# Performance work log

Measured on AMD Instinct MI355X. Metric: run time of the kernel, lower is better.

Reference implementation:

```python
import jax, jax.numpy as jnp
import numpy as np

K, T, RHO, V, TH, EH, S, B = 50, 50, 300, 20000, 800, 200, 10, 256
DELTA = 0.005
LOG_DELTA = float(np.log(DELTA))
EPS = 1e-6


def setup_inputs() -> dict:
    key = jax.random.key(0)
    ks = jax.random.split(key, 32)
    f32 = jnp.float32
    rn = lambda i, shp, s=0.02: jax.random.normal(ks[i], shp, f32) * s
    inp = {
        "unique_tokens": jax.random.randint(ks[0], (100,), 0, V),
        "bows": jax.random.uniform(ks[1], (B, V), f32),
        "normalized_bows": jax.random.uniform(ks[2], (B, V), f32),
        "times": jax.random.randint(ks[3], (B,), 0, T),
        "sources": jax.random.randint(ks[4], (B,), 0, S),
        "rnn_inp": jax.random.normal(ks[5], (S, T, V), f32),
        "num_docs": 100000,
        # learned parameters
        "mu_q_alpha": rn(6, (K, T, RHO), 1.0),
        "logsigma_q_alpha": rn(7, (K, T, RHO), 0.1),
        "rho_W": rn(8, (V, RHO)),                 # Linear(rho_size -> vocab, no bias)
        "W1": rn(9, (TH, V + K)), "b1": jnp.zeros((TH,), f32),
        "W2": rn(10, (TH, TH)), "b2": jnp.zeros((TH,), f32),
        "mu_th_W": rn(11, (K, TH)), "mu_th_b": jnp.zeros((K,), f32),
        "ls_th_W": rn(12, (K, TH)), "ls_th_b": jnp.zeros((K,), f32),
        "eta_map_W": rn(13, (EH, V)), "eta_map_b": jnp.zeros((EH,), f32),
        "lstm_Wih": rn(14, (4 * EH, EH)), "lstm_Whh": rn(15, (4 * EH, EH)),
        "lstm_bih": jnp.zeros((4 * EH,), f32), "lstm_bhh": jnp.zeros((4 * EH,), f32),
        "mu_eta_W": rn(16, (K, EH + K)), "mu_eta_b": jnp.zeros((K,), f32),
        "ls_eta_W": rn(17, (K, EH + K)), "ls_eta_b": jnp.zeros((K,), f32),
        "cls_W": rn(18, (S, K)), "cls_b": jnp.zeros((S,), f32),
    }
    return inp


def _lstm(x_seq, Wih, Whh, bih, bhh):
    # x_seq: [T, S, EH]; torch gate order i,f,g,o
    def step(carry, x):
        h, c = carry
        z = x @ Wih.T + bih + h @ Whh.T + bhh
        i, f, g, o = jnp.split(z, 4, axis=-1)
        c = jax.nn.sigmoid(f) * c + jax.nn.sigmoid(i) * jnp.tanh(g)
        h = jax.nn.sigmoid(o) * jnp.tanh(c)
        return (h, c), h
    h0 = jnp.zeros((x_seq.shape[1], Whh.shape[1]), x_seq.dtype)
    _, out = jax.lax.scan(step, (h0, h0), x_seq)
    return out  # [T, S, EH]


def reference(unique_tokens, bows, normalized_bows, times, sources, rnn_inp, num_docs,
              mu_q_alpha, logsigma_q_alpha, rho_W, W1, b1, W2, b2,
              mu_th_W, mu_th_b, ls_th_W, ls_th_b, eta_map_W, eta_map_b,
              lstm_Wih, lstm_Whh, lstm_bih, lstm_bhh,
              mu_eta_W, mu_eta_b, ls_eta_W, ls_eta_b, cls_W, cls_b):
    # eval-mode semantics: reparameterize returns mu, dropout off
    bsz = bows.shape[0]
    coeff = num_docs / bsz

    # ---- alpha: eval-mode alphas_t == mu_q_alpha[:, t, :]; KL vectorized ----
    mu_a, ls_a = mu_q_alpha, logsigma_q_alpha  # [K, T, RHO]
    kl_a0 = 0.5 * jnp.sum((jnp.exp(ls_a[:, 0]) + mu_a[:, 0] ** 2) / (1.0 + EPS) - 1.0 - ls_a[:, 0])
    diff = mu_a[:, 1:] - mu_a[:, :-1]
    kl_at = 0.5 * jnp.sum((jnp.exp(ls_a[:, 1:]) + diff ** 2) / (DELTA + EPS) - 1.0 + LOG_DELTA - ls_a[:, 1:])
    kl_alpha = kl_a0 + kl_at
    alphas = jnp.transpose(mu_a, (1, 0, 2))  # [T, K, RHO]

    # ---- eta: LSTM over time (vmapped over sources as batch), then recurrence ----
    mapped = jnp.einsum('stv,hv->sth', rnn_inp, eta_map_W) + eta_map_b  # [S, T, EH]
    lstm_out = _lstm(jnp.transpose(mapped, (1, 0, 2)), lstm_Wih, lstm_Whh, lstm_bih, lstm_bhh)  # [T, S, EH]

    inp0 = jnp.concatenate([lstm_out[0], jnp.zeros((S, K), lstm_out.dtype)], axis=-1)
    mu0 = inp0 @ mu_eta_W.T + mu_eta_b
    ls0 = inp0 @ ls_eta_W.T + ls_eta_b  # no clipping at t=0 in original
    kl0 = 0.5 * jnp.sum((jnp.exp(ls0) + mu0 ** 2) / (1.0 + EPS) - 1.0 - ls0)

    def eta_step(carry, out_t):
        eta_prev, kl = carry
        inp_t = jnp.concatenate([out_t, eta_prev], axis=-1)
        mu_t = inp_t @ mu_eta_W.T + mu_eta_b
        ls_t = jnp.clip(inp_t @ ls_eta_W.T + ls_eta_b, -10.0, 10.0)
        kl_t = 0.5 * jnp.sum((jnp.exp(ls_t) + (mu_t - eta_prev) ** 2) / (DELTA + EPS) - 1.0 + LOG_DELTA - ls_t)
        return (mu_t, kl + kl_t), mu_t
    (_, kl_rest), etas_rest = jax.lax.scan(eta_step, (mu0, jnp.float32(0.0)), lstm_out[1:])
    etas = jnp.transpose(jnp.concatenate([mu0[None], etas_rest], axis=0), (1, 0, 2))  # [S, T, K]
    kl_eta = kl0 + kl_rest

    # ---- theta ----
    eta_std = etas[sources, times]  # [B, K]
    h = jax.nn.relu(jnp.concatenate([normalized_bows, eta_std], axis=1) @ W1.T + b1)
    h = jax.nn.relu(h @ W2.T + b2)
    mu_t = h @ mu_th_W.T + mu_th_b
    ls_t = jnp.clip(h @ ls_th_W.T + ls_th_b, -10.0, 10.0)
    theta = jax.nn.softmax(mu_t, axis=-1)
    kl_theta = (0.5 * jnp.sum((jnp.exp(ls_t) + (mu_t - eta_std) ** 2) / (1.0 + EPS) - 1.0 - ls_t)) * coeff

    # ---- beta and NLL ----
    logit = jnp.einsum('tkr,vr->tkv', alphas, rho_W)
    beta = jax.nn.softmax(logit, axis=-1)        # [T, K, V]
    beta_d = beta[times]                         # [B, K, V]
    loglik = jnp.log(jnp.einsum('bk,bkv->bv', theta, beta_d))
    nll = -jnp.sum(loglik * bows) * coeff

    # ---- source prediction loss (sum-reduced cross entropy) ----
    logits = theta @ cls_W.T + cls_b
    logp = jax.nn.log_softmax(logits, axis=-1)
    pred_loss = -jnp.sum(jnp.take_along_axis(logp, sources[:, None], axis=1)) * coeff

    nelbo = nll + kl_alpha + kl_eta + kl_theta + pred_loss
    return (nelbo, nll, kl_alpha, kl_eta, kl_theta, pred_loss)
```

## Files before the change

kernel.cpp:

```cpp
#include <hip/hip_runtime.h>

typedef unsigned int u32;
typedef unsigned short ushort_t;

#define NTOP 50
#define NT_T 50
#define NRHO 300
#define NVOC 20000
#define NTH 800
#define NEH 200
#define NSRC 10
#define NBAT 256

#define OFF_SCAL     0
#define OFF_MAPPED   16
#define OFF_HPRE     100016
#define OFF_H2       304816
#define OFF_Z        509616
#define OFF_DOCCNT   512120
#define OFF_DOCLIST  512176
#define MEMSET_BYTES ((size_t)524976 * 4)
#define OFF_XW       524976
#define OFF_BIAS2    924976
#define OFF_ETAS     925776
#define OFF_WCOEF    950776
#define OFF_W1E      963576
#define OFF_WHH_H    1003576
#define OFF_ETAWH    1083576
#define OFF_H1B      1096376
#define OFF_MAPB     1198776
#define OFF_WIHB     1256120
#define OFF_W2B      1356472
#define OFF_ALPHAB   1714872
#define OFF_RHOB     2124472
#define OFF_NBB      5339832
#define OFF_W1B      7899832
#define OFF_RNNB     16859832
#define OFF_EMWB     21979832
#define OFF_LOGITH   7899832

typedef _Float16 h2v __attribute__((ext_vector_type(2)));
typedef __bf16 bf16x8 __attribute__((ext_vector_type(8)));
typedef float f32x4 __attribute__((ext_vector_type(4)));

#define REP25(M) M(0) M(1) M(2) M(3) M(4) M(5) M(6) M(7) M(8) M(9) M(10) M(11) M(12) \
                 M(13) M(14) M(15) M(16) M(17) M(18) M(19) M(20) M(21) M(22) M(23) M(24)
#define REP7(M) M(0) M(1) M(2) M(3) M(4) M(5) M(6)

__device__ inline float dot2u(u32 a, u32 b, float c){
  h2v ha = __builtin_bit_cast(h2v, a), hb = __builtin_bit_cast(h2v, b);
#if __has_builtin(__builtin_amdgcn_fdot2)
  return __builtin_amdgcn_fdot2(ha, hb, c, false);
#else
  return c + (float)ha.x*(float)hb.x + (float)ha.y*(float)hb.y;
#endif
}

__device__ inline u32 packh2(float lo, float hi){
  h2v h; h.x = (_Float16)lo; h.y = (_Float16)hi;
  return __builtin_bit_cast(u32, h);
}

__device__ inline ushort_t f2bf(float f){
  u32 u = __builtin_bit_cast(u32, f);
  u = (u + 0x7FFFu + ((u >> 16) & 1u)) >> 16;
  return (ushort_t)u;
}

__device__ inline float fast_sig(float x){ return 1.f/(1.f + __expf(-x)); }
__device__ inline float fast_tanh(float x){ float e = __expf(2.f*x); return 1.f - 2.f/(e + 1.f); }

__device__ __forceinline__ void gl2lds16(const void* g, void* l){
  __builtin_amdgcn_global_load_lds((__attribute__((address_space(1))) void*)g,
                                   (__attribute__((address_space(3))) void*)l,
                                   16, 0, 0);
}

__device__ inline void blockReduceAdd(float v, float* red, float* target){
  int tid = threadIdx.x;
  red[tid] = v; __syncthreads();
  for (int o = blockDim.x >> 1; o > 0; o >>= 1){
    if (tid < o) red[tid] += red[tid + o];
    __syncthreads();
  }
  if (tid == 0) atomicAdd(target, red[0]);
}

template<int LDSRC, int MREAL, int KUSED, int KP16>
__device__ inline void conv_row16(const float* __restrict__ src, ushort_t* __restrict__ dst, int i)
{
  int row = i / KP16, cc = i - row*KP16;
  int c = cc*16;
  ushort_t* d = dst + ((size_t)row*KP16 + cc)*16;
  float v[16];
  const float* sr = src + (size_t)row*LDSRC + c;
  if (row < MREAL && c + 16 <= KUSED){
    #pragma unroll
    for (int j = 0; j < 16; j++) v[j] = sr[j];
  } else {
    #pragma unroll
    for (int j = 0; j < 16; j++){
      float x = 0.f;
      if (row < MREAL && c + j < KUSED) x = sr[j];
      v[j] = x;
    }
  }
  ushort_t o[16];
  #pragma unroll
  for (int j = 0; j < 16; j++) o[j] = f2bf(v[j]);
  *(uint4*)d = *(uint4*)o;
  *(uint4*)(d + 8) = *(uint4*)(o + 8);
}

#define P0 64
#define P1 128
#define P2 288
#define P3 416
#define P4 864
#define P5 1120
#define P6 1248
#define P7 1256
#define P8 1272
#define P9 1528
__global__ __launch_bounds__(256) void k_mega(
    const float* __restrict__ whh,
    const float* __restrict__ muEW, const float* __restrict__ lsEW,
    const float* __restrict__ bih, const float* __restrict__ bhh,
    const float* __restrict__ wih, const float* __restrict__ emapB,
    const float* __restrict__ W1, const int* __restrict__ times,
    const float* __restrict__ muq, const float* __restrict__ lsq,
    const float* __restrict__ rho, const float* __restrict__ nb,
    const float* __restrict__ rnn, const float* __restrict__ emapW,
    const float* __restrict__ W2f, float* __restrict__ W)
{
  int b = blockIdx.x, tid = threadIdx.x;
  __shared__ float red[256];
  if (b < P0){
    u32* whhH = (u32*)(W + OFF_WHH_H);
    u32* etaWH = (u32*)(W + OFF_ETAWH);
    for (int idx = b*256 + tid; idx < 133856; idx += P0*256){
      if (idx < 80000){
        int j = idx/100; int i = idx - j*100;
        whhH[idx] = packh2(whh[j*200 + 2*i], whh[j*200 + 2*i + 1]);
      } else if (idx < 92800){
        int d = idx - 80000; int q = d >> 7; int i = d & 127;
        u32 v = 0u;
        if (i < 125){
          const float* src = (q < 50) ? (muEW + q*250) : (lsEW + (q-50)*250);
          v = packh2(src[2*i], src[2*i+1]);
        }
        etaWH[d] = v;
      } else if (idx < 93600){
        int j = idx - 92800;
        float acc = bih[j] + bhh[j];
        const float* wr = wih + (size_t)j*200;
        #pragma unroll 4
        for (int k = 0; k < 200; k++) acc += emapB[k]*wr[k];
        W[OFF_BIAS2 + j] = acc;
      } else if (idx < 133600){
        int d = idx - 93600; int j = d/50; int k = d - j*50;
        W[OFF_W1E + d] = W1[(size_t)j*20050 + 20000 + k];
      } else {
        int bb = idx - 133600; int t = times[bb];
        int* docCnt = (int*)(W + OFF_DOCCNT);
        int* docList = (int*)(W + OFF_DOCLIST);
        int pos = atomicAdd(&docCnt[t], 1);
        docList[t*256 + pos] = bb;
      }
    }
  } else if (b < P1){
    ushort_t* dst = (ushort_t*)(W + OFF_ALPHAB);
    for (int idx = (b-P0)*256 + tid; idx < 102400; idx += (P1-P0)*256){
      int row = idx / 40, c = (idx - row*40) << 3;
      ushort_t out[8];
      const float* src = nullptr;
      if (row < 2500){ int t = row/50, k = row - t*50; src = muq + (size_t)k*15000 + t*300; }
      #pragma unroll
      for (int j = 0; j < 8; j++){
        int r = c + j;
        float v = (src && r < 300) ? src[r] : 0.f;
        out[j] = f2bf(v);
      }
      *(uint4*)(dst + (size_t)row*320 + c) = *(uint4*)out;
    }
  } else if (b < P2){
    ushort_t* dst = (ushort_t*)(W + OFF_RHOB);
    #pragma unroll 2
    for (int i = (b-P1)*256 + tid; i < 20096*20; i += (P2-P1)*256)
      conv_row16<300, 20000, 300, 20>(rho, dst, i);
  } else if (b < P3){
    ushort_t* dst = (ushort_t*)(W + OFF_NBB);
    #pragma unroll 2
    for (int i = (b-P2)*256 + tid; i < 256*1250; i += (P3-P2)*256)
      conv_row16<20000, 256, 20000, 1250>(nb, dst, i);
  } else if (b < P4){
    ushort_t* dst = (ushort_t*)(W + OFF_W1B);
    #pragma unroll 2
    for (int i = (b-P3)*256 + tid; i < 896*1250; i += (P4-P3)*256)
      conv_row16<20050, 800, 20000, 1250>(W1, dst, i);
  } else if (b < P5){
    ushort_t* dst = (ushort_t*)(W + OFF_RNNB);
    #pragma unroll 2
    for (int i = (b-P4)*256 + tid; i < 512*1250; i += (P5-P4)*256)
      conv_row16<20000, 500, 20000, 1250>(rnn, dst, i);
  } else if (b < P6){
    ushort_t* dst = (ushort_t*)(W + OFF_EMWB);
    #pragma unroll 2
    for (int i = (b-P5)*256 + tid; i < 256*1250; i += (P6-P5)*256)
      conv_row16<20000, 200, 20000, 1250>(emapW, dst, i);
  } else if (b < P7){
    ushort_t* dst = (ushort_t*)(W + OFF_WIHB);
    #pragma unroll 2
    for (int i = (b-P6)*256 + tid; i < 896*14; i += (P7-P6)*256)
      conv_row16<200, 800, 200, 14>(wih, dst, i);
  } else if (b < P8){
    ushort_t* dst = (ushort_t*)(W + OFF_W2B);
    #pragma unroll 2
    for (int i = (b-P7)*256 + tid; i < 896*50; i += (P8-P7)*256)
      conv_row16<800, 800, 800, 50>(W2f, dst, i);
  } else {
    const float inv_dl = 1.f/(0.005f + 1e-6f);
    const float logdl = -5.2983173665480363f;
    float local = 0.f;
    for (int idx = (b-P8)*256 + tid; idx < 750000; idx += (P9-P8)*256){
      int rem = idx % 15000; int t = rem / 300;
      float ls = lsq[idx]; float mu = muq[idx];
      if (t == 0){
        local += 0.5f*((__expf(ls) + mu*mu)/(1.f + 1e-6f) - 1.f - ls);
      } else {
        float d = mu - muq[idx - 300];
        local += 0.5f*((__expf(ls) + d*d)*inv_dl - 1.f + logdl - ls);
      }
    }
    blockReduceAdd(local, red, W + OFF_SCAL + 1);
  }
}

__device__ inline void conv_seg(const float* __restrict__ src, int ldsrc,
                                int Mreal, int Kused,
                                ushort_t* __restrict__ dst, int Kp, int idx)
{
  int kb = Kp >> 3;
  int row = idx / kb, c = (idx - row*kb) << 3;
  ushort_t out[8];
  #pragma unroll
  for (int j = 0; j < 8; j++){
    float v = 0.f;
    int k = c + j;
    if (row < Mreal && k < Kused) v = src[(size_t)row*ldsrc + k];
    out[j] = f2bf(v);
  }
  *(uint4*)(dst + (size_t)row*Kp + c) = *(uint4*)out;
}

__global__ __launch_bounds__(256) void k_conv(const float* __restrict__ src, int ldsrc,
                                              int Mreal, int Kused,
                                              ushort_t* __restrict__ dst, int Mp, int Kp)
{
  int idx = blockIdx.x*256 + threadIdx.x;
  int kb = Kp >> 3;
  if (idx >= Mp*kb) return;
  conv_seg(src, ldsrc, Mreal, Kused, dst, Kp, idx);
}

template<int MODE>
__global__ __launch_bounds__(256) void mfma_nt(
    const ushort_t* __restrict__ A, int lda,
    const ushort_t* __restrict__ B, int ldb,
    float* __restrict__ C, _Float16* __restrict__ Ch, int ldc,
    const float* __restrict__ nBias,
    int M, int N, int mT, int kS, int chunks)
{
  __shared__ __align__(16) ushort_t As[2][128*32];
  __shared__ __align__(16) ushort_t Bs[2][128*32];
  int bid = blockIdx.x;
  int kIdx = bid % kS; int rest = bid / kS;
  int mIdx = rest % mT; int nIdx = rest / mT;
  int tid = threadIdx.x;
  int w = tid >> 6, l = tid & 63;
  int c0 = (int)(((long long)chunks * kIdx) / kS);
  int c1 = (int)(((long long)chunks * (kIdx+1)) / kS);
  int r0 = w*32;
  const ushort_t* ga0 = A + (size_t)(mIdx*128 + r0      + (l>>2))*lda + (l&3)*8;
  const ushort_t* ga1 = A + (size_t)(mIdx*128 + r0 + 16 + (l>>2))*lda + (l&3)*8;
  const ushort_t* gb0 = B + (size_t)(nIdx*128 + r0      + (l>>2))*ldb + (l&3)*8;
  const ushort_t* gb1 = B + (size_t)(nIdx*128 + r0 + 16 + (l>>2))*ldb + (l&3)*8;
  int wr = (w >> 1)*64, wc = (w & 1)*64;
  int lr = l & 15, lq = l >> 4;
  f32x4 acc[4][4];
  #pragma unroll
  for (int i = 0; i < 4; i++)
    #pragma unroll
    for (int j = 0; j < 4; j++)
      acc[i][j] = (f32x4)0.f;

  {
    size_t ko = (size_t)c0 * 32;
    gl2lds16(ga0 + ko, As[0] + r0*32);
    gl2lds16(ga1 + ko, As[0] + r0*32 + 512);
    gl2lds16(gb0 + ko, Bs[0] + r0*32);
    gl2lds16(gb1 + ko, Bs[0] + r0*32 + 512);
  }
  asm volatile("s_waitcnt vmcnt(0)" ::: "memory");
  __builtin_amdgcn_s_barrier();

  int cur = 0;
  for (int c = c0; c < c1; c++){
    if (c + 1 < c1){
      size_t ko = (size_t)(c + 1) * 32;
      int nxt = cur ^ 1;
      gl2lds16(ga0 + ko, As[nxt] + r0*32);
      gl2lds16(ga1 + ko, As[nxt] + r0*32 + 512);
      gl2lds16(gb0 + ko, Bs[nxt] + r0*32);
      gl2lds16(gb1 + ko, Bs[nxt] + r0*32 + 512);
    }
    bf16x8 av[4], bv[4];
    #pragma unroll
    for (int i = 0; i < 4; i++)
      av[i] = *(const bf16x8*)(As[cur] + (wr + i*16 + lr)*32 + lq*8);
    #pragma unroll
    for (int j = 0; j < 4; j++)
      bv[j] = *(const bf16x8*)(Bs[cur] + (wc + j*16 + lr)*32 + lq*8);
    #pragma unroll
    for (int i = 0; i < 4; i++)
      #pragma unroll
      for (int j = 0; j < 4; j++)
        acc[i][j] = __builtin_amdgcn_mfma_f32_16x16x32_bf16(av[i], bv[j], acc[i][j], 0, 0, 0);
    asm volatile("s_waitcnt vmcnt(0)" ::: "memory");
    __builtin_amdgcn_s_barrier();
    cur ^= 1;
  }
  if (MODE == 3){
    float* Z = C;
    #pragma unroll
    for (int i = 0; i < 4; i++){
      #pragma unroll
      for (int r = 0; r < 4; r++){
        int row = mIdx*128 + wr + i*16 + lq*4 + r;
        float p = 0.f;
        if (row < M){
          #pragma unroll
          for (int j = 0; j < 4; j++){
            int col = nIdx*128 + wc + j*16 + lr;
            if (col < N){
              float e = __expf(acc[i][j][r]);
              Ch[(size_t)row*ldc + col] = (_Float16)e;
              p += e;
            }
          }
        }
        p += __shfl_xor(p, 1, 16);
        p += __shfl_xor(p, 2, 16);
        p += __shfl_xor(p, 4, 16);
        p += __shfl_xor(p, 8, 16);
        if (lr == 0 && row < M) atomicAdd(&Z[row], p);
      }
    }
  } else {
    #pragma unroll
    for (int i = 0; i < 4; i++){
      #pragma unroll
      for (int r = 0; r < 4; r++){
        int row = mIdx*128 + wr + i*16 + lq*4 + r;
        if (row >= M) continue;
        #pragma unroll
        for (int j = 0; j < 4; j++){
          int col = nIdx*128 + wc + j*16 + lr;
          if (col >= N) continue;
          float v = acc[i][j][r];
          if (MODE == 0)      atomicAdd(&C[(size_t)row*ldc + col], v);
          else                C[(size_t)row*ldc + col] = v + nBias[col];
        }
      }
    }
  }
}

__global__ __launch_bounds__(512, 2) void k_lstm(
    const float* __restrict__ xw, const u32* __restrict__ whhH, const uint4* __restrict__ etaW4,
    const float* __restrict__ muEB, const float* __restrict__ lsEB,
    float* __restrict__ etas, float* __restrict__ W)
{
  int s = blockIdx.x; int tid = threadIdx.x;
  __shared__ uint4 hp4[2][32];
  __shared__ float zbuf[800];
  __shared__ float red[512];
  uint4 z4; z4.x = z4.y = z4.z = z4.w = 0u;
#define DECLW(i) uint4 wa##i = z4, wb##i = z4;
  REP25(DECLW)
#undef DECLW
  float ebias = 0.f;
  if (tid < 400){
    const uint4* ra = (const uint4*)(whhH + tid*100);
    const uint4* rb = (const uint4*)(whhH + (tid + 400)*100);
#define LDW(i) wa##i = ra[i]; wb##i = rb[i];
    REP25(LDW)
#undef LDW
  } else if (tid < 500){
    int q = tid - 400;
    const uint4* re = etaW4 + q*32;
#define LDA(i) wa##i = re[i];
    REP25(LDA)
#undef LDA
#define LDB(i) wb##i = re[25+i];
    REP7(LDB)
#undef LDB
    ebias = (q < 50) ? muEB[q] : lsEB[q - 50];
  }
  float creg = 0.f, muPrev = 0.f, klLocal = 0.f;
  if (tid < 64) ((uint4*)hp4)[tid] = z4;
  __syncthreads();
  const float inv_dl = 1.f/(0.005f + 1e-6f);
  const float logdl = -5.2983173665480363f;

  for (int t = 0; t < NT_T; t++){
    const uint4* hc = hp4[t & 1];
    uint4* hn = hp4[(t + 1) & 1];
    if (tid < 400){
      float a0=0.f,a1=0.f,a2=0.f,a3=0.f,b0=0.f,b1=0.f,b2=0.f,b3=0.f;
#define DOT(i) { uint4 h = hc[i]; \
      a0 = dot2u(wa##i.x, h.x, a0); a1 = dot2u(wa##i.y, h.y, a1); \
      a2 = dot2u(wa##i.z, h.z, a2); a3 = dot2u(wa##i.w, h.w, a3); \
      b0 = dot2u(wb##i.x, h.x, b0); b1 = dot2u(wb##i.y, h.y, b1); \
      b2 = dot2u(wb##i.z, h.z, b2); b3 = dot2u(wb##i.w, h.w, b3); }
      REP25(DOT)
#undef DOT
      const float* xr = xw + (size_t)(s*50 + t)*800;
      zbuf[tid]       = ((a0+a1)+(a2+a3)) + xr[tid];
      zbuf[tid + 400] = ((b0+b1)+(b2+b3)) + xr[tid + 400];
    }
    __syncthreads();
    if (tid < 200){
      float zi = zbuf[tid], zf = zbuf[200+tid], zg = zbuf[400+tid], zo = zbuf[600+tid];
      float ig = fast_sig(zi);
      float fg = fast_sig(zf);
      float gg = fast_tanh(zg);
      float og = fast_sig(zo);
      creg = fg*creg + ig*gg;
      float hv = og*fast_tanh(creg);
      ((_Float16*)hn)[tid] = (_Float16)hv;
    }
    __syncthreads();
    if (tid >= 400 && tid < 500){
      float e0 = ebias, e1 = 0.f, e2 = 0.f, e3 = 0.f;
#define DOTE(i) { uint4 h = hn[i]; \
      e0 = dot2u(wa##i.x, h.x, e0); e1 = dot2u(wa##i.y, h.y, e1); \
      e2 = dot2u(wa##i.z, h.z, e2); e3 = dot2u(wa##i.w, h.w, e3); }
      REP25(DOTE)
#undef DOTE
#define DOTP(i) { uint4 h = hc[25+i]; \
      e0 = dot2u(wb##i.x, h.x, e0); e1 = dot2u(wb##i.y, h.y, e1); \
      e2 = dot2u(wb##i.z, h.z, e2); e3 = dot2u(wb##i.w, h.w, e3); }
      REP7(DOTP)
#undef DOTP
      float eacc = (e0+e1)+(e2+e3);
      int q = tid - 400;
      if (q < 50){
        float mu = eacc;
        etas[(size_t)(s*50 + t)*50 + q] = mu;
        if (t == 0) klLocal += 0.5f*mu*mu/(1.f + 1e-6f);
        else { float d = mu - muPrev; klLocal += 0.5f*d*d*inv_dl; }
        muPrev = mu;
        ((_Float16*)hn)[200 + q] = (_Float16)mu;
      } else {
        float ls = eacc;
        if (t == 0) klLocal += 0.5f*(__expf(ls)/(1.f + 1e-6f) - 1.f - ls);
        else {
          ls = fminf(fmaxf(ls, -10.f), 10.f);
          klLocal += 0.5f*(__expf(ls)*inv_dl - 1.f + logdl - ls);
        }
      }
    }
  }
  __syncthreads();
  blockReduceAdd(klLocal, red, W + OFF_SCAL + 2);
}

__global__ __launch_bounds__(256) void k_h1(
    const float* __restrict__ hpre, const float* __restrict__ b1, const float* __restrict__ w1e,
    const float* __restrict__ etas, const int* __restrict__ times, const int* __restrict__ srcs,
    ushort_t* __restrict__ h1B)
{
  int b = blockIdx.x, tid = threadIdx.x;
  __shared__ float et[50];
  int tb = times[b], sb = srcs[b];
  if (tid < 50) et[tid] = etas[(size_t)(sb*50 + tb)*50 + tid];
  __syncthreads();
  for (int j = tid; j < 800; j += 256){
    float acc = hpre[(size_t)b*800 + j] + b1[j];
    const float* wrow = w1e + (size_t)j*50;
    #pragma unroll
    for (int k = 0; k < 50; k++) acc += et[k]*wrow[k];
    h1B[(size_t)b*800 + j] = f2bf(fmaxf(acc, 0.f));
  }
}

__global__ __launch_bounds__(256) void k_thfin(
    const float* __restrict__ h2g, const float* __restrict__ b2, const float* __restrict__ etas,
    const int* __restrict__ times, const int* __restrict__ srcs,
    const float* __restrict__ muW, const float* __restrict__ muB,
    const float* __restrict__ lsW, const float* __restrict__ lsB,
    const float* __restrict__ clsW, const float* __restrict__ clsB,
    const float* __restrict__ Zrow, float* __restrict__ wcoef, float* __restrict__ W)
{
  int b = blockIdx.x, tid = threadIdx.x;
  __shared__ float h2s[800], mu[50], lsv[50], et[50], th[50], lg[10], red[64], shm[2];
  for (int j = tid; j < 800; j += 256) h2s[j] = fmaxf(h2g[(size_t)b*800 + j] + b2[j], 0.f);
  int tb = times[b], sb = srcs[b];
  if (tid < 50) et[tid] = etas[(size_t)(sb*50 + tb)*50 + tid];
  __syncthreads();
  if (tid < 100){
    int q = (tid < 50) ? tid : tid - 50;
    const float* w = (tid < 50) ? (muW + (size_t)q*800) : (lsW + (size_t)q*800);
    float acc = (tid < 50) ? muB[q] : lsB[q];
    #pragma unroll 8
    for (int j = 0; j < 800; j++) acc += h2s[j]*w[j];
    if (tid < 50) mu[q] = acc;
    else lsv[q] = fminf(fmaxf(acc, -10.f), 10.f);
  }
  __syncthreads();
  if (tid == 0){ float m = -1e30f; for (int k = 0; k < 50; k++) m = fmaxf(m, mu[k]); shm[0] = m; }
  __syncthreads();
  if (tid < 50) th[tid] = __expf(mu[tid] - shm[0]);
  __syncthreads();
  if (tid == 0){ float z = 0.f; for (int k = 0; k < 50; k++) z += th[k]; shm[1] = z; }
  __syncthreads();
  if (tid < 64) red[tid] = 0.f;
  if (tid < 50){
    float t_ = th[tid]/shm[1]; th[tid] = t_;
    wcoef[(size_t)b*50 + tid] = t_/Zrow[tb*50 + tid];
    float d = mu[tid] - et[tid];
    red[tid] = 0.5f*((__expf(lsv[tid]) + d*d)/(1.f + 1e-6f) - 1.f - lsv[tid]);
  }
  __syncthreads();
  if (tid < 10){
    float a = clsB[tid];
    #pragma unroll
    for (int k = 0; k < 50; k++) a += th[k]*clsW[tid*50 + k];
    lg[tid] = a;
  }
  __syncthreads();
  if (tid == 0){
    float m = -1e30f; for (int i = 0; i < 10; i++) m = fmaxf(m, lg[i]);
    float z = 0.f; for (int i = 0; i < 10; i++) z += __expf(lg[i] - m);
    float lse = m + __logf(z);
    atomicAdd(W + OFF_SCAL + 4, lse - lg[sb]);
    float ssum = 0.f; for (int i = 0; i < 50; i++) ssum += red[i];
    atomicAdd(W + OFF_SCAL + 3, ssum);
  }
}

__global__ __launch_bounds__(256) void k_nll(
    const _Float16* __restrict__ E, const float* __restrict__ wcoef,
    const float* __restrict__ bows, float* __restrict__ W)
{
  int t = blockIdx.x/10, vc = blockIdx.x%10;
  int v0 = vc*2000;
  int tid = threadIdx.x;
  const int* docCnt = (const int*)(W + OFF_DOCCNT);
  const int* docList = (const int*)(W + OFF_DOCLIST);
  __shared__ float wch[64*50];
  __shared__ int ids[64];
  __shared__ float red[256];
  int nd = docCnt[t];
  float acc = 0.f;
  for (int d0 = 0; d0 < nd; d0 += 64){
    int ndc = min(64, nd - d0);
    __syncthreads();
    for (int i = tid; i < ndc*50; i += 256){
      int d = i/50, k = i - d*50;
      int bb = docList[t*256 + d0 + d];
      if (k == 0) ids[d] = bb;
      wch[i] = wcoef[(size_t)bb*50 + k];
    }
    __syncthreads();
    for (int v = v0 + tid; v < v0 + 2000; v += 256){
      float e[50];
      #pragma unroll
      for (int k = 0; k < 50; k++)
        e[k] = (float)E[(size_t)(t*50 + k)*NVOC + v];
      for (int d = 0; d < ndc; d++){
        float s = 0.f;
        #pragma unroll
        for (int k = 0; k < 50; k++) s += wch[d*50 + k]*e[k];
        acc += bows[(size_t)ids[d]*NVOC + v]*__logf(s);
      }
    }
  }
  __syncthreads();
  blockReduceAdd(acc, red, W + OFF_SCAL + 0);
}

__global__ void k_final(const float* __restrict__ W, const int* __restrict__ ndocs, float* __restrict__ out)
{
  if (blockIdx.x == 0 && threadIdx.x == 0){
    float coeff = (float)ndocs[0] / 256.f;
    const float* scal = W + OFF_SCAL;
    float nll  = -scal[0]*coeff;
    float kla  = scal[1];
    float kle  = scal[2];
    float klth = scal[3]*coeff;
    float pred = scal[4]*coeff;
    out[0] = nll + kla + kle + klth + pred;
    out[1] = nll; out[2] = kla; out[3] = kle; out[4] = klth; out[5] = pred;
  }
}

extern "C" void kernel_launch(void* const* d_in, const int* in_sizes, int n_in,
                              void* d_out, int out_size, void* d_ws, size_t ws_size,
                              hipStream_t stream)
{
  (void)in_sizes; (void)n_in; (void)out_size; (void)ws_size;
  const float* bows  = (const float*)d_in[1];
  const float* nb    = (const float*)d_in[2];
  const int*   times = (const int*)d_in[3];
  const int*   srcs  = (const int*)d_in[4];
  const float* rnn   = (const float*)d_in[5];
  const int*   ndocs = (const int*)d_in[6];
  const float* muq   = (const float*)d_in[7];
  const float* lsq   = (const float*)d_in[8];
  const float* rho   = (const float*)d_in[9];
  const float* W1    = (const float*)d_in[10];
  const float* b1    = (const float*)d_in[11];
  const float* W2    = (const float*)d_in[12];
  const float* b2    = (const float*)d_in[13];
  const float* muthW = (const float*)d_in[14];
  const float* muthB = (const float*)d_in[15];
  const float* lsthW = (const float*)d_in[16];
  const float* lsthB = (const float*)d_in[17];
  const float* emapW = (const float*)d_in[18];
  const float* emapB = (const float*)d_in[19];
  const float* wih   = (const float*)d_in[20];
  const float* whh   = (const float*)d_in[21];
  const float* bih   = (const float*)d_in[22];
  const float* bhh   = (const float*)d_in[23];
  const float* muEW  = (const float*)d_in[24];
  const float* muEB  = (const float*)d_in[25];
  const float* lsEW  = (const float*)d_in[26];
  const float* lsEB  = (const float*)d_in[27];
  const float* clsW  = (const float*)d_in[28];
  const float* clsB  = (const float*)d_in[29];

  float* W = (float*)d_ws;
  ushort_t* alphaB = (ushort_t*)(W + OFF_ALPHAB);
  ushort_t* rhoB   = (ushort_t*)(W + OFF_RHOB);
  ushort_t* nbB    = (ushort_t*)(W + OFF_NBB);
  ushort_t* w1B    = (ushort_t*)(W + OFF_W1B);
  ushort_t* rnnB   = (ushort_t*)(W + OFF_RNNB);
  ushort_t* emwB   = (ushort_t*)(W + OFF_EMWB);
  ushort_t* wihB   = (ushort_t*)(W + OFF_WIHB);
  ushort_t* w2B    = (ushort_t*)(W + OFF_W2B);
  ushort_t* mapB   = (ushort_t*)(W + OFF_MAPB);
  ushort_t* h1B    = (ushort_t*)(W + OFF_H1B);
  _Float16* Ehalf  = (_Float16*)(W + OFF_LOGITH);

  hipMemsetAsync(d_ws, 0, MEMSET_BYTES, stream);

  k_mega<<<1528, 256, 0, stream>>>(whh, muEW, lsEW, bih, bhh, wih, emapB, W1, times,
                                   muq, lsq, rho, nb, rnn, emapW, W2, W);

  mfma_nt<0><<<4*2*32, 256, 0, stream>>>(
      rnnB, 20000, emwB, 20000, W + OFF_MAPPED, nullptr, 200, nullptr,
      500, 200, 4, 32, 625);

  mfma_nt<0><<<2*7*20, 256, 0, stream>>>(
      nbB, 20000, w1B, 20000, W + OFF_HPRE, nullptr, 800, nullptr,
      256, 800, 2, 20, 625);

  mfma_nt<3><<<20*157, 256, 0, stream>>>(
      alphaB, 320, rhoB, 320, W + OFF_Z, Ehalf, 20000, nullptr,
      2500, 20000, 20, 1, 10);

  k_conv<<<56, 256, 0, stream>>>(W + OFF_MAPPED, 200, 500, 200, mapB, 512, 224);

  mfma_nt<2><<<4*7, 256, 0, stream>>>(
      mapB, 224, wihB, 224, W + OFF_XW, nullptr, 800, W + OFF_BIAS2,
      500, 800, 4, 1, 7);

  k_lstm<<<NSRC, 512, 0, stream>>>(W + OFF_XW, (const u32*)(W + OFF_WHH_H),
                                   (const uint4*)(W + OFF_ETAWH), muEB, lsEB,
                                   W + OFF_ETAS, W);

  k_h1<<<256, 256, 0, stream>>>(W + OFF_HPRE, b1, W + OFF_W1E, W + OFF_ETAS, times, srcs, h1B);

  mfma_nt<0><<<2*7*2, 256, 0, stream>>>(
      h1B, 800, w2B, 800, W + OFF_H2, nullptr, 800, nullptr,
      256, 800, 2, 2, 25);

  k_thfin<<<256, 256, 0, stream>>>(W + OFF_H2, b2, W + OFF_ETAS, times, srcs,
                                   muthW, muthB, lsthW, lsthB, clsW, clsB,
                                   W + OFF_Z, W + OFF_WCOEF, W);

  k_nll<<<500, 256, 0, stream>>>(Ehalf, W + OFF_WCOEF, bows, W);

  k_final<<<1, 64, 0, stream>>>(W, ndocs, (float*)d_out);
}
```

Measured before the change: 697.6 us.

## Co-schedule LSTM recurrence blocks with the beta-logit GEMM in one launch

Merges the serial 10-block LSTM kernel and the large alpha×rho exp-GEMM (Z/Ehalf) into one kernel. The first NSRC blocks run the LSTM and the rest run GEMM tiles, so the long sequential recurrence overlaps with the GEMM instead of leaving most CUs idle. The trade-off is that GEMM blocks now launch as 512-thread blocks with half the threads idle, and they carry the LSTM's register and LDS footprint, which can lower GEMM occupancy.

After: 651.7 us. -6.6%, faster.

```diff
diff --git a/kernel.cpp b/kernel.cpp
--- a/kernel.cpp
+++ b/kernel.cpp
@@ -330,8 +330,183 @@
     __builtin_amdgcn_s_barrier();
     cur ^= 1;
   }
-  if (MODE == 3){
-    float* Z = C;
+  #pragma unroll
+  for (int i = 0; i < 4; i++){
+    #pragma unroll
+    for (int r = 0; r < 4; r++){
+      int row = mIdx*128 + wr + i*16 + lq*4 + r;
+      if (row >= M) continue;
+      #pragma unroll
+      for (int j = 0; j < 4; j++){
+        int col = nIdx*128 + wc + j*16 + lr;
+        if (col >= N) continue;
+        float v = acc[i][j][r];
+        if (MODE == 0)      atomicAdd(&C[(size_t)row*ldc + col], v);
+        else                C[(size_t)row*ldc + col] = v + nBias[col];
+      }
+    }
+  }
+}
+
+__global__ __launch_bounds__(512, 2) void k_fused_lstm_E(
+    const float* __restrict__ xw, const u32* __restrict__ whhH, const uint4* __restrict__ etaW4,
+    const float* __restrict__ muEB, const float* __restrict__ lsEB,
+    float* __restrict__ etas, float* __restrict__ W,
+    const ushort_t* __restrict__ A, const ushort_t* __restrict__ B,
+    _Float16* __restrict__ Ch)
+{
+  __shared__ __align__(16) ushort_t As[2][128*32];
+  __shared__ __align__(16) ushort_t Bs[2][128*32];
+  __shared__ uint4 hp4[2][32];
+  __shared__ float zbuf[800];
+  __shared__ float red[512];
+
+  if (blockIdx.x < NSRC){
+    int s = blockIdx.x; int tid = threadIdx.x;
+    uint4 z4; z4.x = z4.y = z4.z = z4.w = 0u;
+#define DECLW(i) uint4 wa##i = z4, wb##i = z4;
+    REP25(DECLW)
+#undef DECLW
+    float ebias = 0.f;
+    if (tid < 400){
+      const uint4* ra = (const uint4*)(whhH + tid*100);
+      const uint4* rb = (const uint4*)(whhH + (tid + 400)*100);
+#define LDW(i) wa##i = ra[i]; wb##i = rb[i];
+      REP25(LDW)
+#undef LDW
+    } else if (tid < 500){
+      int q = tid - 400;
+      const uint4* re = etaW4 + q*32;
+#define LDA(i) wa##i = re[i];
+      REP25(LDA)
+#undef LDA
+#define LDB(i) wb##i = re[25+i];
+      REP7(LDB)
+#undef LDB
+      ebias = (q < 50) ? muEB[q] : lsEB[q - 50];
+    }
+    float creg = 0.f, muPrev = 0.f, klLocal = 0.f;
+    if (tid < 64) ((uint4*)hp4)[tid] = z4;
+    __syncthreads();
+    const float inv_dl = 1.f/(0.005f + 1e-6f);
+    const float logdl = -5.2983173665480363f;
+
+    for (int t = 0; t < NT_T; t++){
+      const uint4* hc = hp4[t & 1];
+      uint4* hn = hp4[(t + 1) & 1];
+      if (tid < 400){
+        float a0=0.f,a1=0.f,a2=0.f,a3=0.f,b0=0.f,b1=0.f,b2=0.f,b3=0.f;
+#define DOT(i) { uint4 h = hc[i]; \
+        a0 = dot2u(wa##i.x, h.x, a0); a1 = dot2u(wa##i.y, h.y, a1); \
+        a2 = dot2u(wa##i.z, h.z, a2); a3 = dot2u(wa##i.w, h.w, a3); \
+        b0 = dot2u(wb##i.x, h.x, b0); b1 = dot2u(wb##i.y, h.y, b1); \
+        b2 = dot2u(wb##i.z, h.z, b2); b3 = dot2u(wb##i.w, h.w, b3); }
+        REP25(DOT)
+#undef DOT
+        const float* xr = xw + (size_t)(s*50 + t)*800;
+        zbuf[tid]       = ((a0+a1)+(a2+a3)) + xr[tid];
+        zbuf[tid + 400] = ((b0+b1)+(b2+b3)) + xr[tid + 400];
+      }
+      __syncthreads();
+      if (tid < 200){
+        float zi = zbuf[tid], zf = zbuf[200+tid], zg = zbuf[400+tid], zo = zbuf[600+tid];
+        float ig = fast_sig(zi);
+        float fg = fast_sig(zf);
+        float gg = fast_tanh(zg);
+        float og = fast_sig(zo);
+        creg = fg*creg + ig*gg;
+        float hv = og*fast_tanh(creg);
+        ((_Float16*)hn)[tid] = (_Float16)hv;
+      }
+      __syncthreads();
+      if (tid >= 400 && tid < 500){
+        float e0 = ebias, e1 = 0.f, e2 = 0.f, e3 = 0.f;
+#define DOTE(i) { uint4 h = hn[i]; \
+        e0 = dot2u(wa##i.x, h.x, e0); e1 = dot2u(wa##i.y, h.y, e1); \
+        e2 = dot2u(wa##i.z, h.z, e2); e3 = dot2u(wa##i.w, h.w, e3); }
+        REP25(DOTE)
+#undef DOTE
+#define DOTP(i) { uint4 h = hc[25+i]; \
+        e0 = dot2u(wb##i.x, h.x, e0); e1 = dot2u(wb##i.y, h.y, e1); \
+        e2 = dot2u(wb##i.z, h.z, e2); e3 = dot2u(wb##i.w, h.w, e3); }
+        REP7(DOTP)
+#undef DOTP
+        float eacc = (e0+e1)+(e2+e3);
+        int q = tid - 400;
+        if (q < 50){
+          float mu = eacc;
+          etas[(size_t)(s*50 + t)*50 + q] = mu;
+          if (t == 0) klLocal += 0.5f*mu*mu/(1.f + 1e-6f);
+          else { float d = mu - muPrev; klLocal += 0.5f*d*d*inv_dl; }
+          muPrev = mu;
+          ((_Float16*)hn)[200 + q] = (_Float16)mu;
+        } else {
+          float ls = eacc;
+          if (t == 0) klLocal += 0.5f*(__expf(ls)/(1.f + 1e-6f) - 1.f - ls);
+          else {
+            ls = fminf(fmaxf(ls, -10.f), 10.f);
+            klLocal += 0.5f*(__expf(ls)*inv_dl - 1.f + logdl - ls);
+          }
+        }
+      }
+    }
+    __syncthreads();
+    blockReduceAdd(klLocal, red, W + OFF_SCAL + 2);
+  } else {
+    int tid = threadIdx.x;
+    if (tid >= 256) return;
+    int bid = blockIdx.x - NSRC;
+    int mIdx = bid % 20; int nIdx = bid / 20;
+    const int M = 2500, N = 20000, ldc = 20000;
+    int w = tid >> 6, l = tid & 63;
+    int r0 = w*32;
+    const ushort_t* ga0 = A + (size_t)(mIdx*128 + r0      + (l>>2))*320 + (l&3)*8;
+    const ushort_t* ga1 = A + (size_t)(mIdx*128 + r0 + 16 + (l>>2))*320 + (l&3)*8;
+    const ushort_t* gb0 = B + (size_t)(nIdx*128 + r0      + (l>>2))*320 + (l&3)*8;
+    const ushort_t* gb1 = B + (size_t)(nIdx*128 + r0 + 16 + (l>>2))*320 + (l&3)*8;
+    int wr = (w >> 1)*64, wc = (w & 1)*64;
+    int lr = l & 15, lq = l >> 4;
+    f32x4 acc[4][4];
+    #pragma unroll
+    for (int i = 0; i < 4; i++)
+      #pragma unroll
+      for (int j = 0; j < 4; j++)
+        acc[i][j] = (f32x4)0.f;
+
+    gl2lds16(ga0, As[0] + r0*32);
+    gl2lds16(ga1, As[0] + r0*32 + 512);
+    gl2lds16(gb0, Bs[0] + r0*32);
+    gl2lds16(gb1, Bs[0] + r0*32 + 512);
+    asm volatile("s_waitcnt vmcnt(0)" ::: "memory");
+    __builtin_amdgcn_s_barrier();
+
+    int cur = 0;
+    for (int c = 0; c < 10; c++){
+      if (c + 1 < 10){
+        size_t ko = (size_t)(c + 1) * 32;
+        int nxt = cur ^ 1;
+        gl2lds16(ga0 + ko, As[nxt] + r0*32);
+        gl2lds16(ga1 + ko, As[nxt] + r0*32 + 512);
+        gl2lds16(gb0 + ko, Bs[nxt] + r0*32);
+        gl2lds16(gb1 + ko, Bs[nxt] + r0*32 + 512);
+      }
+      bf16x8 av[4], bv[4];
+      #pragma unroll
+      for (int i = 0; i < 4; i++)
+        av[i] = *(const bf16x8*)(As[cur] + (wr + i*16 + lr)*32 + lq*8);
+      #pragma unroll
+      for (int j = 0; j < 4; j++)
+        bv[j] = *(const bf16x8*)(Bs[cur] + (wc + j*16 + lr)*32 + lq*8);
+      #pragma unroll
+      for (int i = 0; i < 4; i++)
+        #pragma unroll
+        for (int j = 0; j < 4; j++)
+          acc[i][j] = __builtin_amdgcn_mfma_f32_16x16x32_bf16(av[i], bv[j], acc[i][j], 0, 0, 0);
+      asm volatile("s_waitcnt vmcnt(0)" ::: "memory");
+      __builtin_amdgcn_s_barrier();
+      cur ^= 1;
+    }
+    float* Z = W + OFF_Z;
     #pragma unroll
     for (int i = 0; i < 4; i++){
       #pragma unroll
@@ -356,124 +531,7 @@
         if (lr == 0 && row < M) atomicAdd(&Z[row], p);
       }
     }
-  } else {
-    #pragma unroll
-    for (int i = 0; i < 4; i++){
-      #pragma unroll
-      for (int r = 0; r < 4; r++){
-        int row = mIdx*128 + wr + i*16 + lq*4 + r;
-        if (row >= M) continue;
-        #pragma unroll
-        for (int j = 0; j < 4; j++){
-          int col = nIdx*128 + wc + j*16 + lr;
-          if (col >= N) continue;
-          float v = acc[i][j][r];
-          if (MODE == 0)      atomicAdd(&C[(size_t)row*ldc + col], v);
-          else                C[(size_t)row*ldc + col] = v + nBias[col];
-        }
-      }
-    }
-  }
-}
-
-__global__ __launch_bounds__(512, 2) void k_lstm(
-    const float* __restrict__ xw, const u32* __restrict__ whhH, const uint4* __restrict__ etaW4,
-    const float* __restrict__ muEB, const float* __restrict__ lsEB,
-    float* __restrict__ etas, float* __restrict__ W)
-{
-  int s = blockIdx.x; int tid = threadIdx.x;
-  __shared__ uint4 hp4[2][32];
-  __shared__ float zbuf[800];
-  __shared__ float red[512];
-  uint4 z4; z4.x = z4.y = z4.z = z4.w = 0u;
-#define DECLW(i) uint4 wa##i = z4, wb##i = z4;
-  REP25(DECLW)
-#undef DECLW
-  float ebias = 0.f;
-  if (tid < 400){
-    const uint4* ra = (const uint4*)(whhH + tid*100);
-    const uint4* rb = (const uint4*)(whhH + (tid + 400)*100);
-#define LDW(i) wa##i = ra[i]; wb##i = rb[i];
-    REP25(LDW)
-#undef LDW
-  } else if (tid < 500){
-    int q = tid - 400;
-    const uint4* re = etaW4 + q*32;
-#define LDA(i) wa##i = re[i];
-    REP25(LDA)
-#undef LDA
-#define LDB(i) wb##i = re[25+i];
-    REP7(LDB)
-#undef LDB
-    ebias = (q < 50) ? muEB[q] : lsEB[q - 50];
-  }
-  float creg = 0.f, muPrev = 0.f, klLocal = 0.f;
-  if (tid < 64) ((uint4*)hp4)[tid] = z4;
-  __syncthreads();
-  const float inv_dl = 1.f/(0.005f + 1e-6f);
-  const float logdl = -5.2983173665480363f;
-
-  for (int t = 0; t < NT_T; t++){
-    const uint4* hc = hp4[t & 1];
-    uint4* hn = hp4[(t + 1) & 1];
-    if (tid < 400){
-      float a0=0.f,a1=0.f,a2=0.f,a3=0.f,b0=0.f,b1=0.f,b2=0.f,b3=0.f;
-#define DOT(i) { uint4 h = hc[i]; \
-      a0 = dot2u(wa##i.x, h.x, a0); a1 = dot2u(wa##i.y, h.y, a1); \
-      a2 = dot2u(wa##i.z, h.z, a2); a3 = dot2u(wa##i.w, h.w, a3); \
-      b0 = dot2u(wb##i.x, h.x, b0); b1 = dot2u(wb##i.y, h.y, b1); \
-      b2 = dot2u(wb##i.z, h.z, b2); b3 = dot2u(wb##i.w, h.w, b3); }
-      REP25(DOT)
-#undef DOT
-      const float* xr = xw + (size_t)(s*50 + t)*800;
-      zbuf[tid]       = ((a0+a1)+(a2+a3)) + xr[tid];
-      zbuf[tid + 400] = ((b0+b1)+(b2+b3)) + xr[tid + 400];
-    }
-    __syncthreads();
-    if (tid < 200){
-      float zi = zbuf[tid], zf = zbuf[200+tid], zg = zbuf[400+tid], zo = zbuf[600+tid];
-      float ig = fast_sig(zi);
-      float fg = fast_sig(zf);
-      float gg = fast_tanh(zg);
-      float og = fast_sig(zo);
-      creg = fg*creg + ig*gg;
-      float hv = og*fast_tanh(creg);
-      ((_Float16*)hn)[tid] = (_Float16)hv;
-    }
-    __syncthreads();
-    if (tid >= 400 && tid < 500){
-      float e0 = ebias, e1 = 0.f, e2 = 0.f, e3 = 0.f;
-#define DOTE(i) { uint4 h = hn[i]; \
-      e0 = dot2u(wa##i.x, h.x, e0); e1 = dot2u(wa##i.y, h.y, e1); \
-      e2 = dot2u(wa##i.z, h.z, e2); e3 = dot2u(wa##i.w, h.w, e3); }
-      REP25(DOTE)
-#undef DOTE
-#define DOTP(i) { uint4 h = hc[25+i]; \
-      e0 = dot2u(wb##i.x, h.x, e0); e1 = dot2u(wb##i.y, h.y, e1); \
-      e2 = dot2u(wb##i.z, h.z, e2); e3 = dot2u(wb##i.w, h.w, e3); }
-      REP7(DOTP)
-#undef DOTP
-      float eacc = (e0+e1)+(e2+e3);
-      int q = tid - 400;
-      if (q < 50){
-        float mu = eacc;
-        etas[(size_t)(s*50 + t)*50 + q] = mu;
-        if (t == 0) klLocal += 0.5f*mu*mu/(1.f + 1e-6f);
-        else { float d = mu - muPrev; klLocal += 0.5f*d*d*inv_dl; }
-        muPrev = mu;
-        ((_Float16*)hn)[200 + q] = (_Float16)mu;
-      } else {
-        float ls = eacc;
-        if (t == 0) klLocal += 0.5f*(__expf(ls)/(1.f + 1e-6f) - 1.f - ls);
-        else {
-          ls = fminf(fmaxf(ls, -10.f), 10.f);
-          klLocal += 0.5f*(__expf(ls)*inv_dl - 1.f + logdl - ls);
-        }
-      }
-    }
-  }
-  __syncthreads();
-  blockReduceAdd(klLocal, red, W + OFF_SCAL + 2);
+  }
 }
 
 __global__ __launch_bounds__(256) void k_h1(
@@ -667,19 +725,15 @@
       nbB, 20000, w1B, 20000, W + OFF_HPRE, nullptr, 800, nullptr,
       256, 800, 2, 20, 625);
 
-  mfma_nt<3><<<20*157, 256, 0, stream>>>(
-      alphaB, 320, rhoB, 320, W + OFF_Z, Ehalf, 20000, nullptr,
-      2500, 20000, 20, 1, 10);
-
   k_conv<<<56, 256, 0, stream>>>(W + OFF_MAPPED, 200, 500, 200, mapB, 512, 224);
 
   mfma_nt<2><<<4*7, 256, 0, stream>>>(
       mapB, 224, wihB, 224, W + OFF_XW, nullptr, 800, W + OFF_BIAS2,
       500, 800, 4, 1, 7);
 
-  k_lstm<<<NSRC, 512, 0, stream>>>(W + OFF_XW, (const u32*)(W + OFF_WHH_H),
-                                   (const uint4*)(W + OFF_ETAWH), muEB, lsEB,
-                                   W + OFF_ETAS, W);
+  k_fused_lstm_E<<<NSRC + 20*157, 512, 0, stream>>>(
+      W + OFF_XW, (const u32*)(W + OFF_WHH_H), (const uint4*)(W + OFF_ETAWH),
+      muEB, lsEB, W + OFF_ETAS, W, alphaB, rhoB, Ehalf);
 
   k_h1<<<256, 256, 0, stream>>>(W + OFF_HPRE, b1, W + OFF_W1E, W + OFF_ETAS, times, srcs, h1B);
 
```
